# Performance work log

Hardware: AMD Instinct MI355X
Metric: run time of the kernel (lower is better)

Reference implementation:

```python
import jax, jax.numpy as jnp
import numpy as np

N_NODES = 50000
N_EDGES = 1_600_000
IN_DIM = 128
OUT_DIM = 128


def setup_inputs() -> dict:
    key = jax.random.key(0)
    k1, k2, k3, k4, k5, k6 = jax.random.split(key, 6)
    H = jax.random.normal(k1, (N_NODES, IN_DIM), dtype=jnp.float32)
    edge_src = jax.random.randint(k2, (N_EDGES,), 0, N_NODES, dtype=jnp.int32)
    edge_dst = jnp.sort(jax.random.randint(k3, (N_EDGES,), 0, N_NODES, dtype=jnp.int32))
    edge_weight = jax.random.uniform(k4, (N_EDGES,), dtype=jnp.float32)
    bound = np.sqrt(6.0 / (IN_DIM + OUT_DIM))
    W = jax.random.uniform(k5, (IN_DIM, OUT_DIM), dtype=jnp.float32, minval=-bound, maxval=bound)
    b = jax.random.normal(k6, (OUT_DIM,), dtype=jnp.float32)
    return {"H": H, "edge_src": edge_src, "edge_dst": edge_dst,
            "edge_weight": edge_weight, "W": W, "b": b}


def reference(H, edge_src, edge_dst, edge_weight, W, b):
    # A_hat @ H: gather source features, scale by edge weight, scatter-sum to dst.
    msgs = edge_weight[:, None] * jnp.take(H, edge_src, axis=0)   # [E, in_dim]
    agg = jax.ops.segment_sum(msgs, edge_dst, num_segments=N_NODES)  # [N, in_dim]
    # Dense transform + bias (no activation in original forward).
    return agg @ W + b
```

## Files before the change

kernel.cpp:

```cpp
#include <hip/hip_runtime.h>

#define IN_DIM 128
#define OUT_DIM 128

typedef __attribute__((ext_vector_type(8))) short short8v;
typedef __attribute__((ext_vector_type(4))) short short4v;
typedef __attribute__((ext_vector_type(4))) float float4v;

__device__ __forceinline__ ushort f2bf(float f) {
    unsigned int u = __builtin_bit_cast(unsigned int, f);
    unsigned int r = (u + 0x7fffu + ((u >> 16) & 1u)) >> 16;
    return (ushort)r;
}
__device__ __forceinline__ float bflo(unsigned int v) {
    return __builtin_bit_cast(float, v << 16);
}
__device__ __forceinline__ float bfhi(unsigned int v) {
    return __builtin_bit_cast(float, v & 0xffff0000u);
}

__global__ __launch_bounds__(256) void prep_kernel(const int* __restrict__ edst,
                                                   int* __restrict__ rp,
                                                   const float* __restrict__ W,
                                                   ushort* __restrict__ Wt,
                                                   int E, int N, int nb_rp) {
    int bid = blockIdx.x;
    if (bid < nb_rp) {
        int n = bid * 256 + threadIdx.x;
        if (n <= N) {
            int lo = 0, hi = E;
            while (lo < hi) {
                int mid = (lo + hi) >> 1;
                if (edst[mid] < n) lo = mid + 1; else hi = mid;
            }
            rp[n] = lo;
        }
    } else {
        int t = threadIdx.x;
        int k0 = (bid - nb_rp) * 8;
        int w = t >> 6, lane = t & 63;
#pragma unroll
        for (int i = 0; i < 2; ++i) {
            int k = k0 + i * 4 + w;
            int n = lane * 2;
            float2 v = *(const float2*)&W[k * 128 + n];
            Wt[n * 136 + k] = f2bf(v.x);
            Wt[(n + 1) * 136 + k] = f2bf(v.y);
        }
    }
}

__global__ __launch_bounds__(256) void gemm_kernel(const float* __restrict__ H,
                                                   const ushort* __restrict__ Wt_g,
                                                   ushort* __restrict__ T, int M) {
    __shared__ ushort Hs[64 * 136];
    __shared__ ushort Ws[128 * 136];

    const int t = threadIdx.x;
    const int row0 = blockIdx.x * 64;

#pragma unroll
    for (int f = t; f < 2176; f += 256)
        ((short8v*)Ws)[f] = ((const short8v*)Wt_g)[f];

#pragma unroll
    for (int i = 0; i < 8; ++i) {
        int r = i * 8 + (t >> 5);
        int c4 = (t & 31) * 4;
        int gr = row0 + r;
        float4 v = make_float4(0.f, 0.f, 0.f, 0.f);
        if (gr < M) v = *(const float4*)&H[gr * 128 + c4];
        short4v o = { (short)f2bf(v.x), (short)f2bf(v.y), (short)f2bf(v.z), (short)f2bf(v.w) };
        *(short4v*)&Hs[r * 136 + c4] = o;
    }
    __syncthreads();

    const int w = t >> 6;
    const int l = t & 63;
    const int m16 = l & 15;
    const int kq = (l >> 4) * 8;

    float4v acc[8];
#pragma unroll
    for (int nt = 0; nt < 8; ++nt) acc[nt] = (float4v){0.f, 0.f, 0.f, 0.f};

#pragma unroll
    for (int ks = 0; ks < 4; ++ks) {
        short8v bfrag = *(const short8v*)&Hs[(w * 16 + m16) * 136 + ks * 32 + kq];
#pragma unroll
        for (int nt = 0; nt < 8; ++nt) {
            short8v afrag = *(const short8v*)&Ws[(nt * 16 + m16) * 136 + ks * 32 + kq];
            acc[nt] = __builtin_amdgcn_mfma_f32_16x16x32_bf16(afrag, bfrag, acc[nt], 0, 0, 0);
        }
    }

    const int gr = row0 + w * 16 + m16;
    if (gr < M) {
        const int q4 = (l >> 4) * 4;
#pragma unroll
        for (int nt = 0; nt < 8; ++nt) {
            short4v o = { (short)f2bf(acc[nt][0]), (short)f2bf(acc[nt][1]),
                          (short)f2bf(acc[nt][2]), (short)f2bf(acc[nt][3]) };
            *(short4v*)&T[gr * 128 + nt * 16 + q4] = o;
        }
    }
}

__global__ __launch_bounds__(256) void scatter_kernel(const unsigned int* __restrict__ T2,
                                                      const int* __restrict__ esrc,
                                                      const float* __restrict__ ew,
                                                      const int* __restrict__ rp,
                                                      const float* __restrict__ b,
                                                      float* __restrict__ out) {
    const int node = blockIdx.x * 4 + (threadIdx.x >> 6);
    const int lane = threadIdx.x & 63;

    const int s = rp[node];
    const int e = rp[node + 1];

    float2 bias = *(const float2*)&b[lane * 2];
    float ax = bias.x, ay = bias.y;

    for (int c = s; c < e; c += 64) {
        int idx = c + lane;
        int srcl = 0;
        float wl = 0.f;
        if (idx < e) { srcl = esrc[idx]; wl = ew[idx]; }
        int nn = e - c;
        if (nn > 64) nn = 64;
        int wli = __builtin_bit_cast(int, wl);
        for (int j = 0; j < nn; j += 4) {
            int s0 = __builtin_amdgcn_readlane(srcl, j + 0);
            int s1 = __builtin_amdgcn_readlane(srcl, j + 1);
            int s2 = __builtin_amdgcn_readlane(srcl, j + 2);
            int s3 = __builtin_amdgcn_readlane(srcl, j + 3);
            float w0 = __builtin_bit_cast(float, __builtin_amdgcn_readlane(wli, j + 0));
            float w1 = __builtin_bit_cast(float, __builtin_amdgcn_readlane(wli, j + 1));
            float w2 = __builtin_bit_cast(float, __builtin_amdgcn_readlane(wli, j + 2));
            float w3 = __builtin_bit_cast(float, __builtin_amdgcn_readlane(wli, j + 3));
            unsigned int v0 = T2[(unsigned int)s0 * 64u + (unsigned int)lane];
            unsigned int v1 = T2[(unsigned int)s1 * 64u + (unsigned int)lane];
            unsigned int v2 = T2[(unsigned int)s2 * 64u + (unsigned int)lane];
            unsigned int v3 = T2[(unsigned int)s3 * 64u + (unsigned int)lane];
            ax += w0 * bflo(v0); ay += w0 * bfhi(v0);
            ax += w1 * bflo(v1); ay += w1 * bfhi(v1);
            ax += w2 * bflo(v2); ay += w2 * bfhi(v2);
            ax += w3 * bflo(v3); ay += w3 * bfhi(v3);
        }
    }

    float2 o = make_float2(ax, ay);
    *(float2*)&out[node * 128 + lane * 2] = o;
}

extern "C" void kernel_launch(void* const* d_in, const int* in_sizes, int n_in,
                              void* d_out, int out_size, void* d_ws, size_t ws_size,
                              hipStream_t stream) {
    const float* H    = (const float*)d_in[0];
    const int*   esrc = (const int*)d_in[1];
    const int*   edst = (const int*)d_in[2];
    const float* ew   = (const float*)d_in[3];
    const float* W    = (const float*)d_in[4];
    const float* b    = (const float*)d_in[5];
    float* out = (float*)d_out;

    const int M = in_sizes[0] / IN_DIM;
    const int E = in_sizes[1];

    ushort* T   = (ushort*)d_ws;
    size_t  off = (size_t)M * 128 * 2;
    ushort* Wt  = (ushort*)((char*)d_ws + off);
    off += 128 * 136 * 2;
    int*    rp  = (int*)((char*)d_ws + off);

    const int nb_rp = (M + 1 + 255) / 256;
    prep_kernel<<<nb_rp + 16, 256, 0, stream>>>(edst, rp, W, Wt, E, M, nb_rp);

    gemm_kernel<<<(M + 63) / 64, 256, 0, stream>>>(H, Wt, T, M);

    scatter_kernel<<<(M + 3) / 4, 256, 0, stream>>>((const unsigned int*)T, esrc, ew, rp, b, out);
}
```

Measured before the change: 160.6 us.

## Load GEMM H fragments directly to registers, pack bf16, unroll scatter by 8

The GEMM kernel no longer stages H through shared memory. Each lane loads its own H fragment straight from global memory into registers and converts it with a packed bf16 conversion, which removes an LDS round trip and part of the sync cost. The W transpose and the output stores now use packed 32-bit bf16 writes. The scatter loop is unrolled from 4 to 8 gathers per step so more loads are in flight. Reads past the last edge read lane entries already zeroed (src 0, weight 0), so they are harmless, but they add wasted gathers for low-degree nodes.

Result: faster. 152.3 us (-5.2%).

```diff
diff --git a/kernel.cpp b/kernel.cpp
--- a/kernel.cpp
+++ b/kernel.cpp
@@ -6,12 +6,24 @@
 typedef __attribute__((ext_vector_type(8))) short short8v;
 typedef __attribute__((ext_vector_type(4))) short short4v;
 typedef __attribute__((ext_vector_type(4))) float float4v;
+typedef __attribute__((ext_vector_type(4))) unsigned int uint4v;
 
 __device__ __forceinline__ ushort f2bf(float f) {
     unsigned int u = __builtin_bit_cast(unsigned int, f);
     unsigned int r = (u + 0x7fffu + ((u >> 16) & 1u)) >> 16;
     return (ushort)r;
 }
+
+__device__ __forceinline__ unsigned int pk2bf(float x, float y) {
+#if __has_builtin(__builtin_amdgcn_cvt_pk_bf16_f32)
+    typedef __attribute__((ext_vector_type(2))) __bf16 bf2;
+    bf2 r = __builtin_amdgcn_cvt_pk_bf16_f32(x, y);
+    return __builtin_bit_cast(unsigned int, r);
+#else
+    return (unsigned int)f2bf(x) | ((unsigned int)f2bf(y) << 16);
+#endif
+}
+
 __device__ __forceinline__ float bflo(unsigned int v) {
     return __builtin_bit_cast(float, v << 16);
 }
@@ -36,16 +48,15 @@
             rp[n] = lo;
         }
     } else {
-        int t = threadIdx.x;
         int k0 = (bid - nb_rp) * 8;
-        int w = t >> 6, lane = t & 63;
-#pragma unroll
-        for (int i = 0; i < 2; ++i) {
-            int k = k0 + i * 4 + w;
-            int n = lane * 2;
-            float2 v = *(const float2*)&W[k * 128 + n];
-            Wt[n * 136 + k] = f2bf(v.x);
-            Wt[(n + 1) * 136 + k] = f2bf(v.y);
+        int n = threadIdx.x & 127;
+        int half = threadIdx.x >> 7;
+#pragma unroll
+        for (int kp = 0; kp < 2; ++kp) {
+            int k = k0 + (half * 2 + kp) * 2;
+            float v0 = W[k * 128 + n];
+            float v1 = W[(k + 1) * 128 + n];
+            *(unsigned int*)&Wt[n * 136 + k] = pk2bf(v0, v1);
         }
     }
 }
@@ -53,7 +64,6 @@
 __global__ __launch_bounds__(256) void gemm_kernel(const float* __restrict__ H,
                                                    const ushort* __restrict__ Wt_g,
                                                    ushort* __restrict__ T, int M) {
-    __shared__ ushort Hs[64 * 136];
     __shared__ ushort Ws[128 * 136];
 
     const int t = threadIdx.x;
@@ -62,23 +72,37 @@
 #pragma unroll
     for (int f = t; f < 2176; f += 256)
         ((short8v*)Ws)[f] = ((const short8v*)Wt_g)[f];
-
-#pragma unroll
-    for (int i = 0; i < 8; ++i) {
-        int r = i * 8 + (t >> 5);
-        int c4 = (t & 31) * 4;
-        int gr = row0 + r;
-        float4 v = make_float4(0.f, 0.f, 0.f, 0.f);
-        if (gr < M) v = *(const float4*)&H[gr * 128 + c4];
-        short4v o = { (short)f2bf(v.x), (short)f2bf(v.y), (short)f2bf(v.z), (short)f2bf(v.w) };
-        *(short4v*)&Hs[r * 136 + c4] = o;
-    }
-    __syncthreads();
 
     const int w = t >> 6;
     const int l = t & 63;
     const int m16 = l & 15;
     const int kq = (l >> 4) * 8;
+    const int gr = row0 + w * 16 + m16;
+
+    float4 h[8];
+    if (gr < M) {
+#pragma unroll
+        for (int ks = 0; ks < 4; ++ks) {
+            h[ks * 2]     = *(const float4*)&H[gr * 128 + ks * 32 + kq];
+            h[ks * 2 + 1] = *(const float4*)&H[gr * 128 + ks * 32 + kq + 4];
+        }
+    } else {
+#pragma unroll
+        for (int i = 0; i < 8; ++i) h[i] = make_float4(0.f, 0.f, 0.f, 0.f);
+    }
+
+    short8v bfrag[4];
+#pragma unroll
+    for (int ks = 0; ks < 4; ++ks) {
+        uint4v u;
+        u[0] = pk2bf(h[ks * 2].x, h[ks * 2].y);
+        u[1] = pk2bf(h[ks * 2].z, h[ks * 2].w);
+        u[2] = pk2bf(h[ks * 2 + 1].x, h[ks * 2 + 1].y);
+        u[3] = pk2bf(h[ks * 2 + 1].z, h[ks * 2 + 1].w);
+        bfrag[ks] = __builtin_bit_cast(short8v, u);
+    }
+
+    __syncthreads();
 
     float4v acc[8];
 #pragma unroll
@@ -86,22 +110,21 @@
 
 #pragma unroll
     for (int ks = 0; ks < 4; ++ks) {
-        short8v bfrag = *(const short8v*)&Hs[(w * 16 + m16) * 136 + ks * 32 + kq];
 #pragma unroll
         for (int nt = 0; nt < 8; ++nt) {
             short8v afrag = *(const short8v*)&Ws[(nt * 16 + m16) * 136 + ks * 32 + kq];
-            acc[nt] = __builtin_amdgcn_mfma_f32_16x16x32_bf16(afrag, bfrag, acc[nt], 0, 0, 0);
-        }
-    }
-
-    const int gr = row0 + w * 16 + m16;
+            acc[nt] = __builtin_amdgcn_mfma_f32_16x16x32_bf16(afrag, bfrag[ks], acc[nt], 0, 0, 0);
+        }
+    }
+
     if (gr < M) {
         const int q4 = (l >> 4) * 4;
 #pragma unroll
         for (int nt = 0; nt < 8; ++nt) {
-            short4v o = { (short)f2bf(acc[nt][0]), (short)f2bf(acc[nt][1]),
-                          (short)f2bf(acc[nt][2]), (short)f2bf(acc[nt][3]) };
-            *(short4v*)&T[gr * 128 + nt * 16 + q4] = o;
+            unsigned int p0 = pk2bf(acc[nt][0], acc[nt][1]);
+            unsigned int p1 = pk2bf(acc[nt][2], acc[nt][3]);
+            uint2 o = make_uint2(p0, p1);
+            *(uint2*)&T[gr * 128 + nt * 16 + q4] = o;
         }
     }
 }
@@ -126,31 +149,31 @@
         int srcl = 0;
         float wl = 0.f;
         if (idx < e) { srcl = esrc[idx]; wl = ew[idx]; }
+        int wli = __builtin_bit_cast(int, wl);
         int nn = e - c;
         if (nn > 64) nn = 64;
-        int wli = __builtin_bit_cast(int, wl);
-        for (int j = 0; j < nn; j += 4) {
-            int s0 = __builtin_amdgcn_readlane(srcl, j + 0);
-            int s1 = __builtin_amdgcn_readlane(srcl, j + 1);
-            int s2 = __builtin_amdgcn_readlane(srcl, j + 2);
-            int s3 = __builtin_amdgcn_readlane(srcl, j + 3);
-            float w0 = __builtin_bit_cast(float, __builtin_amdgcn_readlane(wli, j + 0));
-            float w1 = __builtin_bit_cast(float, __builtin_amdgcn_readlane(wli, j + 1));
-            float w2 = __builtin_bit_cast(float, __builtin_amdgcn_readlane(wli, j + 2));
-            float w3 = __builtin_bit_cast(float, __builtin_amdgcn_readlane(wli, j + 3));
-            unsigned int v0 = T2[(unsigned int)s0 * 64u + (unsigned int)lane];
-            unsigned int v1 = T2[(unsigned int)s1 * 64u + (unsigned int)lane];
-            unsigned int v2 = T2[(unsigned int)s2 * 64u + (unsigned int)lane];
-            unsigned int v3 = T2[(unsigned int)s3 * 64u + (unsigned int)lane];
-            ax += w0 * bflo(v0); ay += w0 * bfhi(v0);
-            ax += w1 * bflo(v1); ay += w1 * bfhi(v1);
-            ax += w2 * bflo(v2); ay += w2 * bfhi(v2);
-            ax += w3 * bflo(v3); ay += w3 * bfhi(v3);
-        }
-    }
-
-    float2 o = make_float2(ax, ay);
-    *(float2*)&out[node * 128 + lane * 2] = o;
+
+        for (int j = 0; j < nn; j += 8) {
+            int ss[8];
+            float ww[8];
+            unsigned int vv[8];
+#pragma unroll
+            for (int q = 0; q < 8; ++q) {
+                ss[q] = __builtin_amdgcn_readlane(srcl, j + q);
+                ww[q] = __builtin_bit_cast(float, __builtin_amdgcn_readlane(wli, j + q));
+            }
+#pragma unroll
+            for (int q = 0; q < 8; ++q)
+                vv[q] = T2[(unsigned int)ss[q] * 64u + (unsigned int)lane];
+#pragma unroll
+            for (int q = 0; q < 8; ++q) {
+                ax += ww[q] * bflo(vv[q]);
+                ay += ww[q] * bfhi(vv[q]);
+            }
+        }
+    }
+
+    *(float2*)&out[node * 128 + lane * 2] = make_float2(ax, ay);
 }
 
 extern "C" void kernel_launch(void* const* d_in, const int* in_sizes, int n_in,
```
